# Kernel tuning notes

Measured on AMD Instinct MI355X. Metric: run time of the kernel, lower is better.

Reference implementation:

```python
import jax, jax.numpy as jnp
import numpy as np

N_NODES = 50000
N_EDGES = 800000
H = 128          # hidden_channels
R = 20           # num_radial
L = 3            # num_layers
CUTOFF = 5.0
N_ATOM_TYPE = 100


def setup_inputs() -> dict:
    key = jax.random.key(0)
    ks = jax.random.split(key, 24)
    z = jax.random.randint(ks[0], (N_NODES,), 0, N_ATOM_TYPE)
    edge_index = jax.random.randint(ks[1], (2, N_EDGES), 0, N_NODES)
    # distances in (0.05, cutoff] so the 1/d term in the RBF stays bounded
    edge_dist = 0.05 + jax.random.uniform(ks[2], (N_EDGES,), jnp.float32) * (CUTOFF - 0.05)
    edge_vec = jax.random.normal(ks[3], (N_EDGES, 3), jnp.float32)
    s = 0.05
    emb = jax.random.normal(ks[4], (N_ATOM_TYPE, H), jnp.float32) * s
    # stacked per-layer params, torch Linear stored as [in, out]
    msg_w1 = jax.random.normal(ks[5], (L, H, H), jnp.float32) * s
    msg_b1 = jnp.zeros((L, H), jnp.float32)
    msg_w2 = jax.random.normal(ks[6], (L, H, 3 * H), jnp.float32) * s
    msg_b2 = jnp.zeros((L, 3 * H), jnp.float32)
    rbf_w = jax.random.normal(ks[7], (L, R, 3 * H), jnp.float32) * s
    rbf_b = jnp.zeros((L, 3 * H), jnp.float32)
    upd_vw = jax.random.normal(ks[8], (L, H, 2 * H), jnp.float32) * s
    upd_w1 = jax.random.normal(ks[9], (L, 2 * H, H), jnp.float32) * s
    upd_b1 = jnp.zeros((L, H), jnp.float32)
    upd_w2 = jax.random.normal(ks[10], (L, H, 3 * H), jnp.float32) * s
    upd_b2 = jnp.zeros((L, 3 * H), jnp.float32)
    out_w1 = jax.random.normal(ks[11], (H, H // 2), jnp.float32) * s
    out_b1 = jnp.zeros((H // 2,), jnp.float32)
    out_w2 = jax.random.normal(ks[12], (H // 2, 1), jnp.float32) * s
    out_b2 = jnp.zeros((1,), jnp.float32)
    return {
        "z": z, "edge_index": edge_index, "edge_dist": edge_dist, "edge_vec": edge_vec,
        "emb": emb,
        "msg_w1": msg_w1, "msg_b1": msg_b1, "msg_w2": msg_w2, "msg_b2": msg_b2,
        "rbf_w": rbf_w, "rbf_b": rbf_b,
        "upd_vw": upd_vw, "upd_w1": upd_w1, "upd_b1": upd_b1,
        "upd_w2": upd_w2, "upd_b2": upd_b2,
        "out_w1": out_w1, "out_b1": out_b1, "out_w2": out_w2, "out_b2": out_b2,
    }


def reference(z, edge_index, edge_dist, edge_vec, emb,
              msg_w1, msg_b1, msg_w2, msg_b2, rbf_w, rbf_b,
              upd_vw, upd_w1, upd_b1, upd_w2, upd_b2,
              out_w1, out_b1, out_w2, out_b2):
    inv_sqrt3 = 1.0 / float(np.sqrt(3.0))
    inv_sqrtH = 1.0 / float(np.sqrt(H))
    inv_sqrt2 = 1.0 / float(np.sqrt(2.0))

    src, dst = edge_index[0], edge_index[1]
    n_nodes = z.shape[0]

    # unit edge direction vectors
    unit = edge_vec / jnp.linalg.norm(edge_vec, axis=-1, keepdims=True)

    # radial basis (RadialBasisLayer)
    d = edge_dist[:, None]                                   # [E,1]
    cosc = 0.5 * (jnp.cos(jnp.pi * edge_dist / CUTOFF) + 1.0)
    cosc = jnp.where(edge_dist <= CUTOFF, cosc, 0.0)         # [E]
    n_idx = jnp.arange(1, R + 1, dtype=edge_dist.dtype)       # [R]
    rbf = (jnp.sin(n_idx * jnp.pi * d / CUTOFF) / d) * cosc[:, None]  # [E,R]

    s = emb[z]                                                # [N,H]
    v = jnp.zeros((n_nodes, 3, H), s.dtype)                   # [N,3,H]

    for l in range(L):
        # --- MessageBlock ---
        mf = jax.nn.silu(s @ msg_w1[l] + msg_b1[l]) @ msg_w2[l] + msg_b2[l]  # [N,3H]
        wf = rbf @ rbf_w[l] + rbf_b[l]                                       # [E,3H]
        prod = mf[src] * wf                                                  # [E,3H]
        w_s, w_vs, w_vv = jnp.split(prod, 3, axis=-1)                        # [E,H] x3
        w_v = v[src] * w_vs[:, None, :] * inv_sqrt3 + w_vv[:, None, :] * unit[:, :, None]  # [E,3,H]
        ds = jax.ops.segment_sum(w_s, dst, num_segments=n_nodes)             # [N,H]
        dv = jax.ops.segment_sum(w_v, dst, num_segments=n_nodes) * inv_sqrtH # [N,3,H]
        s = s + ds
        v = v + dv

        # --- UpdateBlock ---
        vv = v @ upd_vw[l]                                                   # [N,3,2H]
        v1, v2 = jnp.split(vv, 2, axis=-1)                                   # [N,3,H] x2
        v_dot = jnp.einsum('nij,nij->nj', v1, v2) * inv_sqrtH                # [N,H]
        v_norm = jnp.sqrt(jnp.sum(v2 * v2, axis=1) + 1e-12)                  # [N,H]
        feat = jnp.concatenate([s, v_norm], axis=-1)                         # [N,2H]
        uf = jax.nn.silu(feat @ upd_w1[l] + upd_b1[l]) @ upd_w2[l] + upd_b2[l]  # [N,3H]
        a_ss, a_sv, a_v = jnp.split(uf, 3, axis=-1)
        s = s + (v_dot * a_sv + a_ss) * inv_sqrt2
        v = v + v1 * a_v[:, None, :]

    # output MLP + mean readout
    h = jax.nn.silu(s @ out_w1 + out_b1) @ out_w2 + out_b2                   # [N,1]
    return jnp.mean(h, axis=0)                                               # [1]
```

## Files before the change

### kernel.cpp

```cpp
#include <hip/hip_runtime.h>
#include <hip/hip_bf16.h>
#include <math.h>

__device__ __forceinline__ float silu_f(float x) { return x / (1.0f + expf(-x)); }

__global__ __launch_bounds__(256) void k_init_s(const int* __restrict__ z,
                                                const float* __restrict__ emb,
                                                float* __restrict__ s, int total4) {
    int idx = blockIdx.x * 256 + threadIdx.x;
    if (idx < total4) {
        int n = idx >> 5, c4 = idx & 31;
        ((float4*)s)[idx] = ((const float4*)emb)[(size_t)z[n] * 32 + c4];
    }
}

__global__ __launch_bounds__(256) void k_count(const int* __restrict__ ei, int* __restrict__ cnt,
                                               int nE) {
    int e = blockIdx.x * 256 + threadIdx.x;
    if (e < nE) atomicAdd(&cnt[ei[nE + e]], 1);
}

__global__ __launch_bounds__(1024) void k_scan_blk(const int* __restrict__ cnt,
                                                   int* __restrict__ offs,
                                                   int* __restrict__ btot, int N) {
    __shared__ int tmp[1024];
    const int tid = threadIdx.x;
    int i = blockIdx.x * 1024 + tid;
    int val = (i < N) ? cnt[i] : 0;
    tmp[tid] = val;
    __syncthreads();
    for (int off = 1; off < 1024; off <<= 1) {
        int t = (tid >= off) ? tmp[tid - off] : 0;
        __syncthreads();
        tmp[tid] += t;
        __syncthreads();
    }
    if (i < N) offs[i] = tmp[tid] - val;
    if (tid == 1023) btot[blockIdx.x] = tmp[1023];
}

__global__ void k_scan_top(const int* __restrict__ btot, int* __restrict__ btot2,
                           int nb, int* __restrict__ offsN) {
    int tid = threadIdx.x;
    int v = (tid < nb) ? btot[tid] : 0;
    int orig = v;
    #pragma unroll
    for (int off = 1; off < 64; off <<= 1) {
        int u = __shfl_up(v, off, 64);
        if (tid >= off) v += u;
    }
    btot2[tid] = v - orig;
    if (tid == 63) *offsN = v;
}

__global__ __launch_bounds__(256) void k_scan_add(int* __restrict__ offs,
                                                  const int* __restrict__ btot2, int N) {
    int i = blockIdx.x * 256 + threadIdx.x;
    if (i < N) offs[i] += btot2[i >> 10];
}

__global__ __launch_bounds__(256) void k_fill(const int* __restrict__ ei,
                                              const int* __restrict__ offs,
                                              int* __restrict__ cur, int* __restrict__ perm,
                                              int nE) {
    int e = blockIdx.x * 256 + threadIdx.x;
    if (e < nE) {
        int d = ei[nE + e];
        int p = atomicAdd(&cur[d], 1);
        perm[offs[d] + p] = e;
    }
}

__global__ __launch_bounds__(256) void k_prep(const float* __restrict__ edist,
                                              int* __restrict__ perm,
                                              float2* __restrict__ curc2,
                                              int nE, int nEpad) {
    int i = blockIdx.x * 256 + threadIdx.x;
    if (i >= nEpad) return;
    if (i >= nE) { perm[i] = 0; curc2[i] = make_float2(0.f, 0.f); return; }
    int e = perm[i];
    float dd = edist[e];
    float t = 0.62831853071795864769f * dd;
    float cs = cosf(t), sn = sinf(t);
    float cosc = (dd <= 5.0f) ? (0.5f * (cs + 1.0f)) : 0.0f;
    float ic = cosc / dd;
    curc2[i] = make_float2(sn * ic, 2.0f * cs);
}

__global__ __launch_bounds__(256, 4) void k_mf(const float* __restrict__ s,
                                               const float* __restrict__ W1,
                                               const float* __restrict__ b1,
                                               const float* __restrict__ W2,
                                               const float* __restrict__ b2,
                                               float* __restrict__ mf) {
    __shared__ float s_t[16 * 128];
    __shared__ float h_t[16 * 128];
    const int tid = threadIdx.x;
    const size_t nb = (size_t)blockIdx.x * 16;
    {
        const float4* p = (const float4*)(s + nb * 128);
        ((float4*)s_t)[tid] = p[tid];
        ((float4*)s_t)[tid + 256] = p[tid + 256];
    }
    __syncthreads();
    const int c = tid & 127;
    const int g = tid >> 7;
    {
        float acc[8];
        float bb = b1[c];
        #pragma unroll
        for (int i = 0; i < 8; i++) acc[i] = bb;
        for (int k = 0; k < 128; k += 4) {
            float4 sv[8];
            #pragma unroll
            for (int i = 0; i < 8; i++) sv[i] = *(const float4*)&s_t[(g * 8 + i) * 128 + k];
            #pragma unroll
            for (int kk = 0; kk < 4; kk++) {
                float w = W1[(size_t)(k + kk) * 128 + c];
                #pragma unroll
                for (int i = 0; i < 8; i++) acc[i] = fmaf((&sv[i].x)[kk], w, acc[i]);
            }
        }
        #pragma unroll
        for (int i = 0; i < 8; i++) h_t[(g * 8 + i) * 128 + c] = silu_f(acc[i]);
    }
    __syncthreads();
    {
        float acc[8][3];
        #pragma unroll
        for (int q = 0; q < 3; q++) {
            float bb = b2[c + 128 * q];
            #pragma unroll
            for (int i = 0; i < 8; i++) acc[i][q] = bb;
        }
        for (int k = 0; k < 128; k += 4) {
            float4 hv[8];
            #pragma unroll
            for (int i = 0; i < 8; i++) hv[i] = *(const float4*)&h_t[(g * 8 + i) * 128 + k];
            #pragma unroll
            for (int kk = 0; kk < 4; kk++) {
                float w0 = W2[(size_t)(k + kk) * 384 + c];
                float w1 = W2[(size_t)(k + kk) * 384 + c + 128];
                float w2 = W2[(size_t)(k + kk) * 384 + c + 256];
                #pragma unroll
                for (int i = 0; i < 8; i++) {
                    float a = (&hv[i].x)[kk];
                    acc[i][0] = fmaf(a, w0, acc[i][0]);
                    acc[i][1] = fmaf(a, w1, acc[i][1]);
                    acc[i][2] = fmaf(a, w2, acc[i][2]);
                }
            }
        }
        #pragma unroll
        for (int i = 0; i < 8; i++)
            #pragma unroll
            for (int q = 0; q < 3; q++)
                mf[(nb + g * 8 + i) * 384 + c + 128 * q] = acc[i][q];
    }
}

__global__ __launch_bounds__(256, 1) void k_edge5(const int* __restrict__ ei,
                                                  const float* __restrict__ evec,
                                                  const float* __restrict__ mf,
                                                  const float* __restrict__ v,
                                                  const float* __restrict__ Wr,
                                                  const float* __restrict__ br,
                                                  const int* __restrict__ offs,
                                                  const int* __restrict__ perm,
                                                  const float2* __restrict__ curc2,
                                                  float* __restrict__ s,
                                                  float* __restrict__ dV,
                                                  int nN) {
    __shared__ float wrl[8064];
    for (int t = threadIdx.x; t < 8064; t += 256)
        wrl[t] = (t < 7680) ? Wr[t] : br[t - 7680];
    __syncthreads();

    const int lane = threadIdx.x & 63;
    const int wvi = __builtin_amdgcn_readfirstlane(threadIdx.x >> 6);
    const int nbase = blockIdx.x * 16 + wvi * 4;
    const float inv_sqrt3 = 0.57735026918962576451f;

    float brv[6];
    #pragma unroll
    for (int q = 0; q < 6; ++q) brv[q] = wrl[7680 + q * 64 + lane];

    for (int j = 0; j < 4; ++j) {
        const int n = nbase + j;
        if (n >= nN) break;
        const int beg = offs[n], end = offs[n + 1];

        float sa0 = 0.f, sa1 = 0.f;
        float dv00 = 0.f, dv10 = 0.f, dv20 = 0.f;
        float dv01 = 0.f, dv11 = 0.f, dv21 = 0.f;

        for (int i = beg; i < end; i += 4) {
            const int ne = end - i;
            int src[4];
            float ux[4], uy[4], uz[4], cur[4], prev[4], c2v[4];
            #pragma unroll
            for (int t = 0; t < 4; ++t) {
                int e = perm[i + t];
                float2 cc = curc2[i + t];
                cur[t] = cc.x; c2v[t] = cc.y; prev[t] = 0.f;
                src[t] = ei[e];
                float ex = evec[3 * e], ey = evec[3 * e + 1], ez = evec[3 * e + 2];
                float rn = 1.0f / sqrtf(ex * ex + ey * ey + ez * ez);
                ux[t] = ex * rn; uy[t] = ey * rn; uz[t] = ez * rn;
            }
            float gm[4][6], gv[4][6];
            #pragma unroll
            for (int t = 0; t < 4; ++t) {
                const float* mfr = mf + (size_t)src[t] * 384 + lane;
                const float* vr  = v  + (size_t)src[t] * 384 + lane;
                #pragma unroll
                for (int q = 0; q < 6; ++q) { gm[t][q] = mfr[q * 64]; gv[t][q] = vr[q * 64]; }
            }
            float wf[4][6];
            #pragma unroll
            for (int t = 0; t < 4; ++t)
                #pragma unroll
                for (int q = 0; q < 6; ++q) wf[t][q] = brv[q];
            for (int rr = 0; rr < 20; ++rr) {
                float w6[6];
                #pragma unroll
                for (int q = 0; q < 6; ++q) w6[q] = wrl[rr * 384 + q * 64 + lane];
                #pragma unroll
                for (int t = 0; t < 4; ++t) {
                    float c = cur[t];
                    #pragma unroll
                    for (int q = 0; q < 6; ++q) wf[t][q] = fmaf(c, w6[q], wf[t][q]);
                    float nx = fmaf(c2v[t], c, -prev[t]);
                    prev[t] = c; cur[t] = nx;
                }
            }
            #pragma unroll
            for (int t = 0; t < 4; ++t) {
                if (t < ne) {
                    sa0 = fmaf(wf[t][0], gm[t][0], sa0);
                    sa1 = fmaf(wf[t][1], gm[t][1], sa1);
                    float a0 = wf[t][2] * gm[t][2] * inv_sqrt3;
                    float a1 = wf[t][3] * gm[t][3] * inv_sqrt3;
                    float b0 = wf[t][4] * gm[t][4];
                    float b1 = wf[t][5] * gm[t][5];
                    dv00 = fmaf(gv[t][0], a0, fmaf(ux[t], b0, dv00));
                    dv10 = fmaf(gv[t][2], a0, fmaf(uy[t], b0, dv10));
                    dv20 = fmaf(gv[t][4], a0, fmaf(uz[t], b0, dv20));
                    dv01 = fmaf(gv[t][1], a1, fmaf(ux[t], b1, dv01));
                    dv11 = fmaf(gv[t][3], a1, fmaf(uy[t], b1, dv11));
                    dv21 = fmaf(gv[t][5], a1, fmaf(uz[t], b1, dv21));
                }
            }
        }

        float* sp = s + (size_t)n * 128;
        sp[lane] += sa0;
        sp[64 + lane] += sa1;
        float* dp = dV + (size_t)n * 384;
        dp[lane] = dv00;        dp[64 + lane] = dv01;
        dp[128 + lane] = dv10;  dp[192 + lane] = dv11;
        dp[256 + lane] = dv20;  dp[320 + lane] = dv21;
    }
}

__global__ __launch_bounds__(256, 3) void k_upd(float* __restrict__ s,
                                                float* __restrict__ v,
                                                const float* __restrict__ dV,
                                                const float* __restrict__ Wv,
                                                const float* __restrict__ W1,
                                                const float* __restrict__ b1,
                                                const float* __restrict__ W2,
                                                const float* __restrict__ b2) {
    __shared__ float sv[16 * 128];
    __shared__ float vn[16 * 384];
    __shared__ float vnl[16 * 128];
    __shared__ float u1[16 * 128];
    const int tid = threadIdx.x;
    const size_t nb = (size_t)blockIdx.x * 16;
    const float inv_sqrtH = 0.08838834764831845f;
    const float inv_sqrt2 = 0.70710678118654752440f;

    {
        const float4* s4 = (const float4*)(s + nb * 128);
        ((float4*)sv)[tid] = s4[tid];
        ((float4*)sv)[tid + 256] = s4[tid + 256];
        const float4* v4 = (const float4*)(v + nb * 384);
        const float4* e4 = (const float4*)(dV + nb * 384);
        #pragma unroll
        for (int t = 0; t < 6; ++t) {
            float4 av = v4[tid + 256 * t], bv = e4[tid + 256 * t];
            ((float4*)vn)[tid + 256 * t] =
                make_float4(fmaf(bv.x, inv_sqrtH, av.x), fmaf(bv.y, inv_sqrtH, av.y),
                            fmaf(bv.z, inv_sqrtH, av.z), fmaf(bv.w, inv_sqrtH, av.w));
        }
    }
    __syncthreads();
    const int c0 = tid & 63;
    const int ty = tid >> 6;
    float acc[4][3][4];
    {
        #pragma unroll
        for (int i = 0; i < 4; i++)
            #pragma unroll
            for (int d = 0; d < 3; d++)
                #pragma unroll
                for (int cc = 0; cc < 4; cc++) acc[i][d][cc] = 0.f;
        for (int k = 0; k < 128; k += 4) {
            float4 av[4][3];
            #pragma unroll
            for (int i = 0; i < 4; i++)
                #pragma unroll
                for (int d = 0; d < 3; d++)
                    av[i][d] = *(const float4*)&vn[(ty * 4 + i) * 384 + d * 128 + k];
            #pragma unroll
            for (int kk = 0; kk < 4; kk++) {
                float wc[4];
                #pragma unroll
                for (int cc = 0; cc < 4; cc++) wc[cc] = Wv[(size_t)(k + kk) * 256 + c0 + 64 * cc];
                #pragma unroll
                for (int i = 0; i < 4; i++)
                    #pragma unroll
                    for (int d = 0; d < 3; d++) {
                        float a = (&av[i][d].x)[kk];
                        #pragma unroll
                        for (int cc = 0; cc < 4; cc++)
                            acc[i][d][cc] = fmaf(a, wc[cc], acc[i][d][cc]);
                    }
            }
        }
    }
    float vdot[4][2];
    {
        #pragma unroll
        for (int i = 0; i < 4; i++)
            #pragma unroll
            for (int hh = 0; hh < 2; hh++) {
                float d0 = acc[i][0][hh] * acc[i][0][hh + 2] + acc[i][1][hh] * acc[i][1][hh + 2] +
                           acc[i][2][hh] * acc[i][2][hh + 2];
                vdot[i][hh] = d0 * inv_sqrtH;
                float n2 = acc[i][0][hh + 2] * acc[i][0][hh + 2] +
                           acc[i][1][hh + 2] * acc[i][1][hh + 2] +
                           acc[i][2][hh + 2] * acc[i][2][hh + 2];
                vnl[(ty * 4 + i) * 128 + c0 + 64 * hh] = sqrtf(n2 + 1e-12f);
            }
    }
    __syncthreads();
    {
        float a3[4][2];
        float bb0 = b1[c0], bb1 = b1[c0 + 64];
        #pragma unroll
        for (int i = 0; i < 4; i++) { a3[i][0] = bb0; a3[i][1] = bb1; }
        for (int k = 0; k < 128; k += 4) {
            float4 f[4];
            #pragma unroll
            for (int i = 0; i < 4; i++) f[i] = *(const float4*)&sv[(ty * 4 + i) * 128 + k];
            #pragma unroll
            for (int kk = 0; kk < 4; kk++) {
                float w0 = W1[(size_t)(k + kk) * 128 + c0];
                float w1 = W1[(size_t)(k + kk) * 128 + c0 + 64];
                #pragma unroll
                for (int i = 0; i < 4; i++) {
                    float a = (&f[i].x)[kk];
                    a3[i][0] = fmaf(a, w0, a3[i][0]);
                    a3[i][1] = fmaf(a, w1, a3[i][1]);
                }
            }
        }
        for (int k = 0; k < 128; k += 4) {
            float4 f[4];
            #pragma unroll
            for (int i = 0; i < 4; i++) f[i] = *(const float4*)&vnl[(ty * 4 + i) * 128 + k];
            #pragma unroll
            for (int kk = 0; kk < 4; kk++) {
                float w0 = W1[(size_t)(k + kk + 128) * 128 + c0];
                float w1 = W1[(size_t)(k + kk + 128) * 128 + c0 + 64];
                #pragma unroll
                for (int i = 0; i < 4; i++) {
                    float a = (&f[i].x)[kk];
                    a3[i][0] = fmaf(a, w0, a3[i][0]);
                    a3[i][1] = fmaf(a, w1, a3[i][1]);
                }
            }
        }
        #pragma unroll
        for (int i = 0; i < 4; i++) {
            u1[(ty * 4 + i) * 128 + c0] = silu_f(a3[i][0]);
            u1[(ty * 4 + i) * 128 + c0 + 64] = silu_f(a3[i][1]);
        }
    }
    __syncthreads();
    {
        float a4[4][6];
        #pragma unroll
        for (int q = 0; q < 6; q++) {
            float bb = b2[c0 + 64 * q];
            #pragma unroll
            for (int i = 0; i < 4; i++) a4[i][q] = bb;
        }
        for (int k = 0; k < 128; k += 4) {
            float4 uu[4];
            #pragma unroll
            for (int i = 0; i < 4; i++) uu[i] = *(const float4*)&u1[(ty * 4 + i) * 128 + k];
            #pragma unroll
            for (int kk = 0; kk < 4; kk++) {
                float w[6];
                #pragma unroll
                for (int q = 0; q < 6; q++) w[q] = W2[(size_t)(k + kk) * 384 + c0 + 64 * q];
                #pragma unroll
                for (int i = 0; i < 4; i++) {
                    float a = (&uu[i].x)[kk];
                    #pragma unroll
                    for (int q = 0; q < 6; q++) a4[i][q] = fmaf(a, w[q], a4[i][q]);
                }
            }
        }
        #pragma unroll
        for (int i = 0; i < 4; i++) {
            int node = ty * 4 + i;
            size_t nr = nb + node;
            #pragma unroll
            for (int hh = 0; hh < 2; ++hh) {
                int h = c0 + 64 * hh;
                float a_ss = a4[i][hh], a_sv = a4[i][2 + hh], a_v = a4[i][4 + hh];
                s[nr * 128 + h] = sv[node * 128 + h] + (vdot[i][hh] * a_sv + a_ss) * inv_sqrt2;
                #pragma unroll
                for (int d = 0; d < 3; ++d)
                    v[nr * 384 + d * 128 + h] =
                        vn[node * 384 + d * 128 + h] + acc[i][d][hh] * a_v;
            }
        }
    }
}

__global__ __launch_bounds__(256, 4) void k_out(const float* __restrict__ s,
                                                const float* __restrict__ ow1,
                                                const float* __restrict__ ob1,
                                                const float* __restrict__ ow2,
                                                const float* __restrict__ ob2,
                                                float* __restrict__ out, int nNodes) {
    __shared__ float st[16 * 128];
    __shared__ float red[4];
    const int tid = threadIdx.x;
    const size_t nb = (size_t)blockIdx.x * 16;
    {
        const float4* p = (const float4*)(s + nb * 128);
        ((float4*)st)[tid] = p[tid];
        ((float4*)st)[tid + 256] = p[tid + 256];
    }
    __syncthreads();
    const int c = tid & 63;
    const int ty = tid >> 6;
    float acc[4];
    float bb = ob1[c];
    #pragma unroll
    for (int i = 0; i < 4; i++) acc[i] = bb;
    for (int k = 0; k < 128; k += 4) {
        float4 sv[4];
        #pragma unroll
        for (int i = 0; i < 4; i++) sv[i] = *(const float4*)&st[(ty * 4 + i) * 128 + k];
        #pragma unroll
        for (int kk = 0; kk < 4; kk++) {
            float w = ow1[(size_t)(k + kk) * 64 + c];
            #pragma unroll
            for (int i = 0; i < 4; i++) acc[i] = fmaf((&sv[i].x)[kk], w, acc[i]);
        }
    }
    float w2 = ow2[c];
    float p = 0.f;
    #pragma unroll
    for (int i = 0; i < 4; i++) p += silu_f(acc[i]) * w2;
    #pragma unroll
    for (int off = 32; off > 0; off >>= 1) p += __shfl_down(p, off, 64);
    if (c == 0) red[ty] = p;
    __syncthreads();
    if (tid == 0) {
        float val = (red[0] + red[1] + red[2] + red[3]) * (1.0f / (float)nNodes);
        if (blockIdx.x == 0) val += ob2[0];
        atomicAdd(out, val);
    }
}

extern "C" void kernel_launch(void* const* d_in, const int* in_sizes, int n_in,
                              void* d_out, int out_size, void* d_ws, size_t ws_size,
                              hipStream_t stream) {
    const int*   z     = (const int*)d_in[0];
    const int*   ei    = (const int*)d_in[1];
    const float* edist = (const float*)d_in[2];
    const float* evec  = (const float*)d_in[3];
    const float* emb   = (const float*)d_in[4];
    const float* mw1   = (const float*)d_in[5];
    const float* mb1   = (const float*)d_in[6];
    const float* mw2   = (const float*)d_in[7];
    const float* mb2   = (const float*)d_in[8];
    const float* rw    = (const float*)d_in[9];
    const float* rbb   = (const float*)d_in[10];
    const float* uvw   = (const float*)d_in[11];
    const float* uw1   = (const float*)d_in[12];
    const float* ub1   = (const float*)d_in[13];
    const float* uw2   = (const float*)d_in[14];
    const float* ub2   = (const float*)d_in[15];
    const float* ow1   = (const float*)d_in[16];
    const float* ob1   = (const float*)d_in[17];
    const float* ow2   = (const float*)d_in[18];
    const float* ob2   = (const float*)d_in[19];

    const int N = in_sizes[0];
    const int E = in_sizes[2];
    const int Ep = E + 4;

    const size_t need = ((size_t)N * 1280 + (N + 1) + Ep) * 4 + (size_t)Ep * 8;
    hipMemsetAsync(d_out, 0, out_size * sizeof(float), stream);
    if (ws_size < need) return;

    float* ws = (float*)d_ws;
    float*  s     = ws;
    float*  v     = s + (size_t)N * 128;
    float*  mf    = v + (size_t)N * 384;
    float*  dV    = mf + (size_t)N * 384;
    int*    offs  = (int*)(dV + (size_t)N * 384);
    int*    perm  = offs + (N + 1);
    float2* curc2 = (float2*)(perm + Ep);
    int*    cnt   = (int*)curc2;
    int*    cur   = cnt + N;
    int*    btot  = cur + N;
    int*    btot2 = btot + 64;

    hipMemsetAsync(v, 0, (size_t)N * 384 * sizeof(float), stream);
    hipMemsetAsync(cnt, 0, (size_t)2 * N * sizeof(int), stream);

    const int nbScan = (N + 1023) / 1024;
    k_count<<<(E + 255) / 256, 256, 0, stream>>>(ei, cnt, E);
    k_scan_blk<<<nbScan, 1024, 0, stream>>>(cnt, offs, btot, N);
    k_scan_top<<<1, 64, 0, stream>>>(btot, btot2, nbScan, offs + N);
    k_scan_add<<<(N + 255) / 256, 256, 0, stream>>>(offs, btot2, N);
    k_fill<<<(E + 255) / 256, 256, 0, stream>>>(ei, offs, cur, perm, E);
    k_prep<<<(Ep + 255) / 256, 256, 0, stream>>>(edist, perm, curc2, E, Ep);

    k_init_s<<<(N * 32 + 255) / 256, 256, 0, stream>>>(z, emb, s, N * 32);

    for (int l = 0; l < 3; ++l) {
        k_mf<<<N / 16, 256, 0, stream>>>(s, mw1 + (size_t)l * 16384, mb1 + l * 128,
                                         mw2 + (size_t)l * 49152, mb2 + l * 384, mf);
        k_edge5<<<(N + 15) / 16, 256, 0, stream>>>(ei, evec, mf, v,
                                                   rw + (size_t)l * 7680, rbb + l * 384,
                                                   offs, perm, curc2, s, dV, N);
        k_upd<<<N / 16, 256, 0, stream>>>(s, v, dV, uvw + (size_t)l * 32768,
                                          uw1 + (size_t)l * 32768, ub1 + l * 128,
                                          uw2 + (size_t)l * 49152, ub2 + l * 384);
    }
    k_out<<<N / 16, 256, 0, stream>>>(s, ow1, ob1, ow2, ob2, (float*)d_out, N);
}
```

Baseline: 2.790 ms.

## Interleave message features and vector state per node for edge gathers

Stores the per-node message features and the vector features next to each other in one 768-float row, so each edge gather reads one contiguous 3 KB region instead of two separate 1.5 KB rows. The mf, edge and update kernels are changed to use the interleaved stride. The edge kernel also handles 8 nodes per wave (32 per block) instead of 4, which halves the number of blocks and the per-block shared-memory loads of the RBF weights, at the cost of fewer blocks for load balancing.

```diff
diff --git a/kernel.cpp b/kernel.cpp
--- a/kernel.cpp
+++ b/kernel.cpp
@@ -92,7 +92,7 @@
                                                const float* __restrict__ b1,
                                                const float* __restrict__ W2,
                                                const float* __restrict__ b2,
-                                               float* __restrict__ mf) {
+                                               float* __restrict__ mfv) {
     __shared__ float s_t[16 * 128];
     __shared__ float h_t[16 * 128];
     const int tid = threadIdx.x;
@@ -155,14 +155,13 @@
         for (int i = 0; i < 8; i++)
             #pragma unroll
             for (int q = 0; q < 3; q++)
-                mf[(nb + g * 8 + i) * 384 + c + 128 * q] = acc[i][q];
-    }
-}
-
-__global__ __launch_bounds__(256, 1) void k_edge5(const int* __restrict__ ei,
+                mfv[(nb + g * 8 + i) * 768 + c + 128 * q] = acc[i][q];
+    }
+}
+
+__global__ __launch_bounds__(256, 1) void k_edge7(const int* __restrict__ ei,
                                                   const float* __restrict__ evec,
-                                                  const float* __restrict__ mf,
-                                                  const float* __restrict__ v,
+                                                  const float* __restrict__ mfv,
                                                   const float* __restrict__ Wr,
                                                   const float* __restrict__ br,
                                                   const int* __restrict__ offs,
@@ -178,14 +177,14 @@
 
     const int lane = threadIdx.x & 63;
     const int wvi = __builtin_amdgcn_readfirstlane(threadIdx.x >> 6);
-    const int nbase = blockIdx.x * 16 + wvi * 4;
+    const int nbase = blockIdx.x * 32 + wvi * 8;
     const float inv_sqrt3 = 0.57735026918962576451f;
 
     float brv[6];
     #pragma unroll
     for (int q = 0; q < 6; ++q) brv[q] = wrl[7680 + q * 64 + lane];
 
-    for (int j = 0; j < 4; ++j) {
+    for (int j = 0; j < 8; ++j) {
         const int n = nbase + j;
         if (n >= nN) break;
         const int beg = offs[n], end = offs[n + 1];
@@ -211,10 +210,9 @@
             float gm[4][6], gv[4][6];
             #pragma unroll
             for (int t = 0; t < 4; ++t) {
-                const float* mfr = mf + (size_t)src[t] * 384 + lane;
-                const float* vr  = v  + (size_t)src[t] * 384 + lane;
-                #pragma unroll
-                for (int q = 0; q < 6; ++q) { gm[t][q] = mfr[q * 64]; gv[t][q] = vr[q * 64]; }
+                const float* base = mfv + (size_t)src[t] * 768 + lane;
+                #pragma unroll
+                for (int q = 0; q < 6; ++q) { gm[t][q] = base[q * 64]; gv[t][q] = base[384 + q * 64]; }
             }
             float wf[4][6];
             #pragma unroll
@@ -264,7 +262,7 @@
 }
 
 __global__ __launch_bounds__(256, 3) void k_upd(float* __restrict__ s,
-                                                float* __restrict__ v,
+                                                float* __restrict__ mfv,
                                                 const float* __restrict__ dV,
                                                 const float* __restrict__ Wv,
                                                 const float* __restrict__ W1,
@@ -284,12 +282,15 @@
         const float4* s4 = (const float4*)(s + nb * 128);
         ((float4*)sv)[tid] = s4[tid];
         ((float4*)sv)[tid + 256] = s4[tid + 256];
-        const float4* v4 = (const float4*)(v + nb * 384);
-        const float4* e4 = (const float4*)(dV + nb * 384);
+        const int nd = tid >> 4;
+        const int cl = tid & 15;
+        const float4* vbase = (const float4*)(mfv + (nb + nd) * 768 + 384);
+        const float4* ebase = (const float4*)(dV + (nb + nd) * 384);
         #pragma unroll
         for (int t = 0; t < 6; ++t) {
-            float4 av = v4[tid + 256 * t], bv = e4[tid + 256 * t];
-            ((float4*)vn)[tid + 256 * t] =
+            int idx = cl + 16 * t;
+            float4 av = vbase[idx], bv = ebase[idx];
+            ((float4*)vn)[nd * 96 + idx] =
                 make_float4(fmaf(bv.x, inv_sqrtH, av.x), fmaf(bv.y, inv_sqrtH, av.y),
                             fmaf(bv.z, inv_sqrtH, av.z), fmaf(bv.w, inv_sqrtH, av.w));
         }
@@ -425,7 +426,7 @@
                 s[nr * 128 + h] = sv[node * 128 + h] + (vdot[i][hh] * a_sv + a_ss) * inv_sqrt2;
                 #pragma unroll
                 for (int d = 0; d < 3; ++d)
-                    v[nr * 384 + d * 128 + h] =
+                    mfv[nr * 768 + 384 + d * 128 + h] =
                         vn[node * 384 + d * 128 + h] + acc[i][d][hh] * a_v;
             }
         }
@@ -514,9 +515,8 @@
 
     float* ws = (float*)d_ws;
     float*  s     = ws;
-    float*  v     = s + (size_t)N * 128;
-    float*  mf    = v + (size_t)N * 384;
-    float*  dV    = mf + (size_t)N * 384;
+    float*  mfv   = s + (size_t)N * 128;
+    float*  dV    = mfv + (size_t)N * 768;
     int*    offs  = (int*)(dV + (size_t)N * 384);
     int*    perm  = offs + (N + 1);
     float2* curc2 = (float2*)(perm + Ep);
@@ -525,7 +525,7 @@
     int*    btot  = cur + N;
     int*    btot2 = btot + 64;
 
-    hipMemsetAsync(v, 0, (size_t)N * 384 * sizeof(float), stream);
+    hipMemsetAsync(mfv, 0, (size_t)N * 768 * sizeof(float), stream);
     hipMemsetAsync(cnt, 0, (size_t)2 * N * sizeof(int), stream);
 
     const int nbScan = (N + 1023) / 1024;
@@ -540,11 +540,11 @@
 
     for (int l = 0; l < 3; ++l) {
         k_mf<<<N / 16, 256, 0, stream>>>(s, mw1 + (size_t)l * 16384, mb1 + l * 128,
-                                         mw2 + (size_t)l * 49152, mb2 + l * 384, mf);
-        k_edge5<<<(N + 15) / 16, 256, 0, stream>>>(ei, evec, mf, v,
+                                         mw2 + (size_t)l * 49152, mb2 + l * 384, mfv);
+        k_edge7<<<(N + 31) / 32, 256, 0, stream>>>(ei, evec, mfv,
                                                    rw + (size_t)l * 7680, rbb + l * 384,
                                                    offs, perm, curc2, s, dV, N);
-        k_upd<<<N / 16, 256, 0, stream>>>(s, v, dV, uvw + (size_t)l * 32768,
+        k_upd<<<N / 16, 256, 0, stream>>>(s, mfv, dV, uvw + (size_t)l * 32768,
                                           uw1 + (size_t)l * 32768, ub1 + l * 128,
                                           uw2 + (size_t)l * 49152, ub2 + l * 384);
     }
```

New measurement: 2.927 ms. 1.05x slower.

## Fuse next layer's message MLP and output MLP into update kernel

Applied to the files above, without the earlier changes.

The per-node update kernel now also computes the next layer's message MLP (mf) from the freshly updated s held in shared memory, and the last layer's update is fused with the output MLP and mean readout. This removes re-reading s from global memory and saves three kernel launches. The last layer also skips writing s and v back to global memory. In exchange the fused kernels carry more work per block and need extra barriers, which may raise register pressure and lower occupancy.

```diff
diff --git a/kernel.cpp b/kernel.cpp
--- a/kernel.cpp
+++ b/kernel.cpp
@@ -263,14 +263,19 @@
     }
 }
 
-__global__ __launch_bounds__(256, 3) void k_upd(float* __restrict__ s,
-                                                float* __restrict__ v,
-                                                const float* __restrict__ dV,
-                                                const float* __restrict__ Wv,
-                                                const float* __restrict__ W1,
-                                                const float* __restrict__ b1,
-                                                const float* __restrict__ W2,
-                                                const float* __restrict__ b2) {
+__global__ __launch_bounds__(256, 3) void k_updmf(float* __restrict__ s,
+                                                  float* __restrict__ v,
+                                                  const float* __restrict__ dV,
+                                                  const float* __restrict__ Wv,
+                                                  const float* __restrict__ W1,
+                                                  const float* __restrict__ b1,
+                                                  const float* __restrict__ W2,
+                                                  const float* __restrict__ b2,
+                                                  const float* __restrict__ W1m,
+                                                  const float* __restrict__ b1m,
+                                                  const float* __restrict__ W2m,
+                                                  const float* __restrict__ b2m,
+                                                  float* __restrict__ mf) {
     __shared__ float sv[16 * 128];
     __shared__ float vn[16 * 384];
     __shared__ float vnl[16 * 128];
@@ -414,6 +419,7 @@
                 }
             }
         }
+        __syncthreads();
         #pragma unroll
         for (int i = 0; i < 4; i++) {
             int node = ty * 4 + i;
@@ -422,7 +428,9 @@
             for (int hh = 0; hh < 2; ++hh) {
                 int h = c0 + 64 * hh;
                 float a_ss = a4[i][hh], a_sv = a4[i][2 + hh], a_v = a4[i][4 + hh];
-                s[nr * 128 + h] = sv[node * 128 + h] + (vdot[i][hh] * a_sv + a_ss) * inv_sqrt2;
+                float snew = sv[node * 128 + h] + (vdot[i][hh] * a_sv + a_ss) * inv_sqrt2;
+                s[nr * 128 + h] = snew;
+                sv[node * 128 + h] = snew;
                 #pragma unroll
                 for (int d = 0; d < 3; ++d)
                     v[nr * 384 + d * 128 + h] =
@@ -430,53 +438,262 @@
             }
         }
     }
-}
-
-__global__ __launch_bounds__(256, 4) void k_out(const float* __restrict__ s,
-                                                const float* __restrict__ ow1,
-                                                const float* __restrict__ ob1,
-                                                const float* __restrict__ ow2,
-                                                const float* __restrict__ ob2,
-                                                float* __restrict__ out, int nNodes) {
-    __shared__ float st[16 * 128];
+    __syncthreads();
+    const int c = tid & 127;
+    const int g = tid >> 7;
+    {
+        float am[8];
+        float bb = b1m[c];
+        #pragma unroll
+        for (int i = 0; i < 8; i++) am[i] = bb;
+        for (int k = 0; k < 128; k += 4) {
+            float4 svv[8];
+            #pragma unroll
+            for (int i = 0; i < 8; i++) svv[i] = *(const float4*)&sv[(g * 8 + i) * 128 + k];
+            #pragma unroll
+            for (int kk = 0; kk < 4; kk++) {
+                float w = W1m[(size_t)(k + kk) * 128 + c];
+                #pragma unroll
+                for (int i = 0; i < 8; i++) am[i] = fmaf((&svv[i].x)[kk], w, am[i]);
+            }
+        }
+        #pragma unroll
+        for (int i = 0; i < 8; i++) u1[(g * 8 + i) * 128 + c] = silu_f(am[i]);
+    }
+    __syncthreads();
+    {
+        float am[8][3];
+        #pragma unroll
+        for (int q = 0; q < 3; q++) {
+            float bb = b2m[c + 128 * q];
+            #pragma unroll
+            for (int i = 0; i < 8; i++) am[i][q] = bb;
+        }
+        for (int k = 0; k < 128; k += 4) {
+            float4 hv[8];
+            #pragma unroll
+            for (int i = 0; i < 8; i++) hv[i] = *(const float4*)&u1[(g * 8 + i) * 128 + k];
+            #pragma unroll
+            for (int kk = 0; kk < 4; kk++) {
+                float w0 = W2m[(size_t)(k + kk) * 384 + c];
+                float w1 = W2m[(size_t)(k + kk) * 384 + c + 128];
+                float w2 = W2m[(size_t)(k + kk) * 384 + c + 256];
+                #pragma unroll
+                for (int i = 0; i < 8; i++) {
+                    float a = (&hv[i].x)[kk];
+                    am[i][0] = fmaf(a, w0, am[i][0]);
+                    am[i][1] = fmaf(a, w1, am[i][1]);
+                    am[i][2] = fmaf(a, w2, am[i][2]);
+                }
+            }
+        }
+        #pragma unroll
+        for (int i = 0; i < 8; i++)
+            #pragma unroll
+            for (int q = 0; q < 3; q++)
+                mf[(nb + g * 8 + i) * 384 + c + 128 * q] = am[i][q];
+    }
+}
+
+__global__ __launch_bounds__(256, 3) void k_updout(const float* __restrict__ s,
+                                                   const float* __restrict__ v,
+                                                   const float* __restrict__ dV,
+                                                   const float* __restrict__ Wv,
+                                                   const float* __restrict__ W1,
+                                                   const float* __restrict__ b1,
+                                                   const float* __restrict__ W2,
+                                                   const float* __restrict__ b2,
+                                                   const float* __restrict__ ow1,
+                                                   const float* __restrict__ ob1,
+                                                   const float* __restrict__ ow2,
+                                                   const float* __restrict__ ob2,
+                                                   float* __restrict__ out, int nNodes) {
+    __shared__ float sv[16 * 128];
+    __shared__ float vn[16 * 384];
+    __shared__ float vnl[16 * 128];
+    __shared__ float u1[16 * 128];
     __shared__ float red[4];
     const int tid = threadIdx.x;
     const size_t nb = (size_t)blockIdx.x * 16;
-    {
-        const float4* p = (const float4*)(s + nb * 128);
-        ((float4*)st)[tid] = p[tid];
-        ((float4*)st)[tid + 256] = p[tid + 256];
-    }
-    __syncthreads();
-    const int c = tid & 63;
+    const float inv_sqrtH = 0.08838834764831845f;
+    const float inv_sqrt2 = 0.70710678118654752440f;
+
+    {
+        const float4* s4 = (const float4*)(s + nb * 128);
+        ((float4*)sv)[tid] = s4[tid];
+        ((float4*)sv)[tid + 256] = s4[tid + 256];
+        const float4* v4 = (const float4*)(v + nb * 384);
+        const float4* e4 = (const float4*)(dV + nb * 384);
+        #pragma unroll
+        for (int t = 0; t < 6; ++t) {
+            float4 av = v4[tid + 256 * t], bv = e4[tid + 256 * t];
+            ((float4*)vn)[tid + 256 * t] =
+                make_float4(fmaf(bv.x, inv_sqrtH, av.x), fmaf(bv.y, inv_sqrtH, av.y),
+                            fmaf(bv.z, inv_sqrtH, av.z), fmaf(bv.w, inv_sqrtH, av.w));
+        }
+    }
+    __syncthreads();
+    const int c0 = tid & 63;
     const int ty = tid >> 6;
-    float acc[4];
-    float bb = ob1[c];
-    #pragma unroll
-    for (int i = 0; i < 4; i++) acc[i] = bb;
-    for (int k = 0; k < 128; k += 4) {
-        float4 sv[4];
-        #pragma unroll
-        for (int i = 0; i < 4; i++) sv[i] = *(const float4*)&st[(ty * 4 + i) * 128 + k];
-        #pragma unroll
-        for (int kk = 0; kk < 4; kk++) {
-            float w = ow1[(size_t)(k + kk) * 64 + c];
-            #pragma unroll
-            for (int i = 0; i < 4; i++) acc[i] = fmaf((&sv[i].x)[kk], w, acc[i]);
-        }
-    }
-    float w2 = ow2[c];
-    float p = 0.f;
-    #pragma unroll
-    for (int i = 0; i < 4; i++) p += silu_f(acc[i]) * w2;
-    #pragma unroll
-    for (int off = 32; off > 0; off >>= 1) p += __shfl_down(p, off, 64);
-    if (c == 0) red[ty] = p;
-    __syncthreads();
-    if (tid == 0) {
-        float val = (red[0] + red[1] + red[2] + red[3]) * (1.0f / (float)nNodes);
-        if (blockIdx.x == 0) val += ob2[0];
-        atomicAdd(out, val);
+    float acc[4][3][4];
+    {
+        #pragma unroll
+        for (int i = 0; i < 4; i++)
+            #pragma unroll
+            for (int d = 0; d < 3; d++)
+                #pragma unroll
+                for (int cc = 0; cc < 4; cc++) acc[i][d][cc] = 0.f;
+        for (int k = 0; k < 128; k += 4) {
+            float4 av[4][3];
+            #pragma unroll
+            for (int i = 0; i < 4; i++)
+                #pragma unroll
+                for (int d = 0; d < 3; d++)
+                    av[i][d] = *(const float4*)&vn[(ty * 4 + i) * 384 + d * 128 + k];
+            #pragma unroll
+            for (int kk = 0; kk < 4; kk++) {
+                float wc[4];
+                #pragma unroll
+                for (int cc = 0; cc < 4; cc++) wc[cc] = Wv[(size_t)(k + kk) * 256 + c0 + 64 * cc];
+                #pragma unroll
+                for (int i = 0; i < 4; i++)
+                    #pragma unroll
+                    for (int d = 0; d < 3; d++) {
+                        float a = (&av[i][d].x)[kk];
+                        #pragma unroll
+                        for (int cc = 0; cc < 4; cc++)
+                            acc[i][d][cc] = fmaf(a, wc[cc], acc[i][d][cc]);
+                    }
+            }
+        }
+    }
+    float vdot[4][2];
+    {
+        #pragma unroll
+        for (int i = 0; i < 4; i++)
+            #pragma unroll
+            for (int hh = 0; hh < 2; hh++) {
+                float d0 = acc[i][0][hh] * acc[i][0][hh + 2] + acc[i][1][hh] * acc[i][1][hh + 2] +
+                           acc[i][2][hh] * acc[i][2][hh + 2];
+                vdot[i][hh] = d0 * inv_sqrtH;
+                float n2 = acc[i][0][hh + 2] * acc[i][0][hh + 2] +
+                           acc[i][1][hh + 2] * acc[i][1][hh + 2] +
+                           acc[i][2][hh + 2] * acc[i][2][hh + 2];
+                vnl[(ty * 4 + i) * 128 + c0 + 64 * hh] = sqrtf(n2 + 1e-12f);
+            }
+    }
+    __syncthreads();
+    {
+        float a3[4][2];
+        float bb0 = b1[c0], bb1 = b1[c0 + 64];
+        #pragma unroll
+        for (int i = 0; i < 4; i++) { a3[i][0] = bb0; a3[i][1] = bb1; }
+        for (int k = 0; k < 128; k += 4) {
+            float4 f[4];
+            #pragma unroll
+            for (int i = 0; i < 4; i++) f[i] = *(const float4*)&sv[(ty * 4 + i) * 128 + k];
+            #pragma unroll
+            for (int kk = 0; kk < 4; kk++) {
+                float w0 = W1[(size_t)(k + kk) * 128 + c0];
+                float w1 = W1[(size_t)(k + kk) * 128 + c0 + 64];
+                #pragma unroll
+                for (int i = 0; i < 4; i++) {
+                    float a = (&f[i].x)[kk];
+                    a3[i][0] = fmaf(a, w0, a3[i][0]);
+                    a3[i][1] = fmaf(a, w1, a3[i][1]);
+                }
+            }
+        }
+        for (int k = 0; k < 128; k += 4) {
+            float4 f[4];
+            #pragma unroll
+            for (int i = 0; i < 4; i++) f[i] = *(const float4*)&vnl[(ty * 4 + i) * 128 + k];
+            #pragma unroll
+            for (int kk = 0; kk < 4; kk++) {
+                float w0 = W1[(size_t)(k + kk + 128) * 128 + c0];
+                float w1 = W1[(size_t)(k + kk + 128) * 128 + c0 + 64];
+                #pragma unroll
+                for (int i = 0; i < 4; i++) {
+                    float a = (&f[i].x)[kk];
+                    a3[i][0] = fmaf(a, w0, a3[i][0]);
+                    a3[i][1] = fmaf(a, w1, a3[i][1]);
+                }
+            }
+        }
+        #pragma unroll
+        for (int i = 0; i < 4; i++) {
+            u1[(ty * 4 + i) * 128 + c0] = silu_f(a3[i][0]);
+            u1[(ty * 4 + i) * 128 + c0 + 64] = silu_f(a3[i][1]);
+        }
+    }
+    __syncthreads();
+    {
+        float a4[4][6];
+        #pragma unroll
+        for (int q = 0; q < 6; q++) {
+            float bb = b2[c0 + 64 * q];
+            #pragma unroll
+            for (int i = 0; i < 4; i++) a4[i][q] = bb;
+        }
+        for (int k = 0; k < 128; k += 4) {
+            float4 uu[4];
+            #pragma unroll
+            for (int i = 0; i < 4; i++) uu[i] = *(const float4*)&u1[(ty * 4 + i) * 128 + k];
+            #pragma unroll
+            for (int kk = 0; kk < 4; kk++) {
+                float w[6];
+                #pragma unroll
+                for (int q = 0; q < 6; q++) w[q] = W2[(size_t)(k + kk) * 384 + c0 + 64 * q];
+                #pragma unroll
+                for (int i = 0; i < 4; i++) {
+                    float a = (&uu[i].x)[kk];
+                    #pragma unroll
+                    for (int q = 0; q < 6; q++) a4[i][q] = fmaf(a, w[q], a4[i][q]);
+                }
+            }
+        }
+        __syncthreads();
+        #pragma unroll
+        for (int i = 0; i < 4; i++) {
+            int node = ty * 4 + i;
+            #pragma unroll
+            for (int hh = 0; hh < 2; ++hh) {
+                int h = c0 + 64 * hh;
+                sv[node * 128 + h] = sv[node * 128 + h] +
+                                     (vdot[i][hh] * a4[i][2 + hh] + a4[i][hh]) * inv_sqrt2;
+            }
+        }
+    }
+    __syncthreads();
+    {
+        float ao[4];
+        float bb = ob1[c0];
+        #pragma unroll
+        for (int i = 0; i < 4; i++) ao[i] = bb;
+        for (int k = 0; k < 128; k += 4) {
+            float4 f[4];
+            #pragma unroll
+            for (int i = 0; i < 4; i++) f[i] = *(const float4*)&sv[(ty * 4 + i) * 128 + k];
+            #pragma unroll
+            for (int kk = 0; kk < 4; kk++) {
+                float w = ow1[(size_t)(k + kk) * 64 + c0];
+                #pragma unroll
+                for (int i = 0; i < 4; i++) ao[i] = fmaf((&f[i].x)[kk], w, ao[i]);
+            }
+        }
+        float w2 = ow2[c0];
+        float p = 0.f;
+        #pragma unroll
+        for (int i = 0; i < 4; i++) p += silu_f(ao[i]) * w2;
+        #pragma unroll
+        for (int off = 32; off > 0; off >>= 1) p += __shfl_down(p, off, 64);
+        if (c0 == 0) red[ty] = p;
+        __syncthreads();
+        if (tid == 0) {
+            float val = (red[0] + red[1] + red[2] + red[3]) * (1.0f / (float)nNodes);
+            if (blockIdx.x == 0) val += ob2[0];
+            atomicAdd(out, val);
+        }
     }
 }
 
@@ -537,16 +754,24 @@
     k_prep<<<(Ep + 255) / 256, 256, 0, stream>>>(edist, perm, curc2, E, Ep);
 
     k_init_s<<<(N * 32 + 255) / 256, 256, 0, stream>>>(z, emb, s, N * 32);
+    k_mf<<<N / 16, 256, 0, stream>>>(s, mw1, mb1, mw2, mb2, mf);
 
     for (int l = 0; l < 3; ++l) {
-        k_mf<<<N / 16, 256, 0, stream>>>(s, mw1 + (size_t)l * 16384, mb1 + l * 128,
-                                         mw2 + (size_t)l * 49152, mb2 + l * 384, mf);
         k_edge5<<<(N + 15) / 16, 256, 0, stream>>>(ei, evec, mf, v,
                                                    rw + (size_t)l * 7680, rbb + l * 384,
                                                    offs, perm, curc2, s, dV, N);
-        k_upd<<<N / 16, 256, 0, stream>>>(s, v, dV, uvw + (size_t)l * 32768,
-                                          uw1 + (size_t)l * 32768, ub1 + l * 128,
-                                          uw2 + (size_t)l * 49152, ub2 + l * 384);
-    }
-    k_out<<<N / 16, 256, 0, stream>>>(s, ow1, ob1, ow2, ob2, (float*)d_out, N);
-}
+        if (l < 2) {
+            k_updmf<<<N / 16, 256, 0, stream>>>(s, v, dV, uvw + (size_t)l * 32768,
+                                                uw1 + (size_t)l * 32768, ub1 + l * 128,
+                                                uw2 + (size_t)l * 49152, ub2 + l * 384,
+                                                mw1 + (size_t)(l + 1) * 16384, mb1 + (l + 1) * 128,
+                                                mw2 + (size_t)(l + 1) * 49152, mb2 + (l + 1) * 384,
+                                                mf);
+        } else {
+            k_updout<<<N / 16, 256, 0, stream>>>(s, v, dV, uvw + (size_t)l * 32768,
+                                                 uw1 + (size_t)l * 32768, ub1 + l * 128,
+                                                 uw2 + (size_t)l * 49152, ub2 + l * 384,
+                                                 ow1, ob1, ow2, ob2, (float*)d_out, N);
+        }
+    }
+}
```

New measurement: 2.752 ms. Within noise of the previous version (-1.4%).
